# Performance work log

Measured on AMD Instinct MI355X. Metric: run time of the kernel, lower is better.

## Reference

```python
import jax, jax.numpy as jnp
import numpy as np

N, LATENT, HIDDEN, OUT, B = 65536, 128, 512, 64, 1024
W_WIDTH = 4.0  # LSH bucket width params['w']


def setup_inputs() -> dict:
    key = jax.random.key(0)
    ks = jax.random.split(key, 6)
    return {
        "z": jax.random.normal(ks[0], (N, LATENT), jnp.float32),
        "W1": jax.random.normal(ks[1], (LATENT, HIDDEN), jnp.float32) / np.float32(np.sqrt(LATENT)),
        "b1": jnp.zeros((HIDDEN,), jnp.float32),
        "W2": jax.random.normal(ks[2], (HIDDEN, OUT), jnp.float32) / np.float32(np.sqrt(HIDDEN)),
        "b2": jnp.zeros((OUT,), jnp.float32),
        "a": jax.random.normal(ks[3], (OUT,), jnp.float32),
        "lsh_b": jax.random.uniform(ks[4], (1,), jnp.float32) * W_WIDTH,
    }


def reference(z, W1, b1, W2, b2, a, lsh_b):
    # decoder MLP: latent -> hidden (relu) -> output_dim
    h = jax.nn.relu(z @ W1 + b1)
    x = h @ W2 + b2                                     # [N, OUT]
    # LSH random-projection hash: floor((x.a + b)/w), bucketed mod B
    code = jnp.floor((x @ a + lsh_b[0]) / W_WIDTH)
    bucket = jnp.mod(code.astype(jnp.int32), B)         # [N] segment ids
    # dict-based cluster grouping -> segmented mean per hash bucket
    sums = jax.ops.segment_sum(x, bucket, num_segments=B)                # [B, OUT]
    counts = jax.ops.segment_sum(jnp.ones((x.shape[0],), x.dtype), bucket, num_segments=B)
    means = sums / jnp.maximum(counts, 1.0)[:, None]    # [B, OUT]
    # squared distances point -> every cluster mean (gram trick, no [N,B,OUT] tensor)
    d2 = jnp.maximum(
        jnp.sum(x * x, -1)[:, None] + jnp.sum(means * means, -1)[None, :]
        - 2.0 * (x @ means.T),
        0.0)                                            # [N, B]
    # DEC-style Student-t soft cluster assignment
    q = 1.0 / (1.0 + d2)
    q_s = q / jnp.sum(q, -1, keepdims=True)
    return (q_s, means)
```

## Files before the change

### kernel.cpp

```cpp
#include <hip/hip_runtime.h>
#include <hip/hip_bf16.h>

#define N_PTS   65536
#define LATENT  128
#define HIDDEN  512
#define OUT_D   64
#define NBUCKET 1024
#define ROWS_A  32

typedef __attribute__((ext_vector_type(8))) short frag_ab;
typedef __attribute__((ext_vector_type(4))) float f32x4;

__device__ __forceinline__ short bf16h(float f) {
    union { float f; unsigned u; } c; c.f = f;
    const unsigned r = (c.u + 0x7FFFu + ((c.u >> 16) & 1u)) >> 16;
    return (short)r;
}
__device__ __forceinline__ float bf16tof(short s) {
    union { unsigned u; float f; } c; c.u = ((unsigned)(unsigned short)s) << 16;
    return c.f;
}

__global__ __launch_bounds__(256) void prep_weights(
    const float* __restrict__ W1, const float* __restrict__ W2,
    short* __restrict__ wfrag)
{
    const int tid = blockIdx.x * 256 + threadIdx.x;
    const int c = tid / 1536;
    const int u = tid % 1536;
    frag_ab hi, lo;
    if (u < 1024) {
        const int l = u >> 4, slot = u & 15;
        const int j = slot ^ (l & 7);
        const int ct = j >> 3, ks = (j >> 1) & 3, hl = j & 1;
        const int n = (c * 2 + ct) * 16 + (l & 15);
        const int k0 = ks * 32 + ((l >> 4) << 3);
#pragma unroll
        for (int e = 0; e < 8; ++e) {
            const float wv = W1[(size_t)(k0 + e) * HIDDEN + n];
            const short h = bf16h(wv);
            hi[e] = h;
            lo[e] = bf16h(wv - bf16tof(h));
        }
        ((frag_ab*)wfrag)[(size_t)c * 1536 + u] = hl ? lo : hi;
    } else {
        const int u2 = u - 1024;
        const int l = u2 >> 3, slot = u2 & 7;
        const int j = slot ^ (l & 7);
        const int ot = j >> 1, hl = j & 1;
        const int n = ot * 16 + (l & 15);
#pragma unroll
        for (int e = 0; e < 8; ++e) {
            const int k = c * 32 + ((e >> 2) << 4) + ((l >> 4) << 2) + (e & 3);
            const float wv = W2[(size_t)k * OUT_D + n];
            const short h = bf16h(wv);
            hi[e] = h;
            lo[e] = bf16h(wv - bf16tof(h));
        }
        ((frag_ab*)wfrag)[(size_t)c * 1536 + u] = hl ? lo : hi;
    }
}

#define BAND_U   5e-4f

__global__ __launch_bounds__(256, 2) void mlp_mfma_kernel(
    const float* __restrict__ z, const short* __restrict__ wfrag,
    const float* __restrict__ b1, const float* __restrict__ b2,
    const float* __restrict__ a, const float* __restrict__ lsh_b,
    float* __restrict__ x_out, float* __restrict__ xnorm_out,
    int* __restrict__ bucket_out, int* __restrict__ wsflag)
{
    __shared__ frag_ab LD[3072];
    float* LDf = (float*)LD;
    float4* LDf4 = (float4*)LD;
    const int t = threadIdx.x;
    const int l = t & 63, w = t >> 6;
    const int sw = l & 7;
    const int row0 = blockIdx.x * 128 + w * 32;
    const frag_ab* wg = (const frag_ab*)wfrag;

    frag_ab zh[2][4], zl[2][4];
#pragma unroll
    for (int rg = 0; rg < 2; ++rg)
#pragma unroll
        for (int ks = 0; ks < 4; ++ks) {
            const float* src = z + (size_t)(row0 + rg * 16 + (l & 15)) * LATENT
                             + ks * 32 + ((l >> 4) << 3);
            const float4 p0 = *(const float4*)src;
            const float4 p1 = *(const float4*)(src + 4);
            const float v[8] = {p0.x, p0.y, p0.z, p0.w, p1.x, p1.y, p1.z, p1.w};
#pragma unroll
            for (int e = 0; e < 8; ++e) {
                const short h = bf16h(v[e]);
                zh[rg][ks][e] = h;
                zl[rg][ks][e] = bf16h(v[e] - bf16tof(h));
            }
        }

    f32x4 acc2[2][4];
#pragma unroll
    for (int rg = 0; rg < 2; ++rg)
#pragma unroll
        for (int ot = 0; ot < 4; ++ot) acc2[rg][ot] = (f32x4){0.f, 0.f, 0.f, 0.f};

#pragma unroll
    for (int i = 0; i < 6; ++i)
        __builtin_amdgcn_global_load_lds(
            (const __attribute__((address_space(1))) void*)(wg + (w * 6 + i) * 64 + l),
            (__attribute__((address_space(3))) void*)(&LD[(w * 6 + i) * 64]),
            16, 0, 0);
    __syncthreads();

#pragma unroll 1
    for (int c = 0; c < 16; ++c) {
        const int pb = (c & 1) * 1536;
        const int sb = 1536 - pb;
        if (c < 15) {
#pragma unroll
            for (int i = 0; i < 6; ++i)
                __builtin_amdgcn_global_load_lds(
                    (const __attribute__((address_space(1))) void*)(wg + (size_t)(c + 1) * 1536 + (w * 6 + i) * 64 + l),
                    (__attribute__((address_space(3))) void*)(&LD[sb + (w * 6 + i) * 64]),
                    16, 0, 0);
        }

        f32x4 acc1[2][2];
#pragma unroll
        for (int ct_l = 0; ct_l < 2; ++ct_l) {
            frag_ab bh[4], bl[4];
#pragma unroll
            for (int ks = 0; ks < 4; ++ks) {
                bh[ks] = LD[pb + l * 16 + ct_l * 8 + ((ks * 2) ^ sw)];
                bl[ks] = LD[pb + l * 16 + ct_l * 8 + ((ks * 2 + 1) ^ sw)];
            }
#pragma unroll
            for (int rg = 0; rg < 2; ++rg) {
                f32x4 acc = (f32x4){0.f, 0.f, 0.f, 0.f};
#pragma unroll
                for (int ks = 0; ks < 4; ++ks) {
                    acc = __builtin_amdgcn_mfma_f32_16x16x32_bf16(bh[ks], zh[rg][ks], acc, 0, 0, 0);
                    acc = __builtin_amdgcn_mfma_f32_16x16x32_bf16(bl[ks], zh[rg][ks], acc, 0, 0, 0);
                    acc = __builtin_amdgcn_mfma_f32_16x16x32_bf16(bh[ks], zl[rg][ks], acc, 0, 0, 0);
                }
                acc1[ct_l][rg] = acc;
            }
        }

        float4 b1v[2];
#pragma unroll
        for (int ct_l = 0; ct_l < 2; ++ct_l)
            b1v[ct_l] = *(const float4*)&b1[(c * 2 + ct_l) * 16 + ((l >> 4) << 2)];
        frag_ab ah2[2], al2[2];
#pragma unroll
        for (int rg = 0; rg < 2; ++rg)
#pragma unroll
            for (int e = 0; e < 8; ++e) {
                const int tile = e >> 2, r = e & 3;
                const float bb = (r == 0) ? b1v[tile].x : (r == 1) ? b1v[tile].y
                               : (r == 2) ? b1v[tile].z : b1v[tile].w;
                const float hv = fmaxf(acc1[tile][rg][r] + bb, 0.f);
                const short hh = bf16h(hv);
                ah2[rg][e] = hh;
                al2[rg][e] = bf16h(hv - bf16tof(hh));
            }

#pragma unroll
        for (int ot = 0; ot < 4; ++ot) {
            const frag_ab b2h = LD[pb + 1024 + l * 8 + ((ot * 2) ^ sw)];
            const frag_ab b2l = LD[pb + 1024 + l * 8 + ((ot * 2 + 1) ^ sw)];
#pragma unroll
            for (int rg = 0; rg < 2; ++rg) {
                acc2[rg][ot] = __builtin_amdgcn_mfma_f32_16x16x32_bf16(ah2[rg], b2h, acc2[rg][ot], 0, 0, 0);
                acc2[rg][ot] = __builtin_amdgcn_mfma_f32_16x16x32_bf16(al2[rg], b2h, acc2[rg][ot], 0, 0, 0);
                acc2[rg][ot] = __builtin_amdgcn_mfma_f32_16x16x32_bf16(ah2[rg], b2l, acc2[rg][ot], 0, 0, 0);
            }
        }
        __syncthreads();
    }

    float b2v[4], av[4];
#pragma unroll
    for (int ot = 0; ot < 4; ++ot) {
        b2v[ot] = b2[ot * 16 + (l & 15)];
        av[ot]  = a[ot * 16 + (l & 15)];
    }
    const int pbase = w * 512;
    int flagged = 0;
    const float lb = lsh_b[0];
#pragma unroll
    for (int rg = 0; rg < 2; ++rg)
#pragma unroll
        for (int r = 0; r < 4; ++r) {
            float sp = 0.f, np = 0.f;
            const int row_l = rg * 16 + (l >> 4) * 4 + r;
#pragma unroll
            for (int ot = 0; ot < 4; ++ot) {
                const float xv = acc2[rg][ot][r] + b2v[ot];
                sp = fmaf(xv, av[ot], sp);
                np = fmaf(xv, xv, np);
                const int col = ot * 16 + (l & 15);
                LDf[pbase * 4 + row_l * 64 + col] = xv;
            }
#pragma unroll
            for (int off = 8; off >= 1; off >>= 1) {
                sp += __shfl_xor(sp, off, 16);
                np += __shfl_xor(np, off, 16);
            }
            if ((l & 15) == 0) {
                const int row = row0 + row_l;
                const float v = sp + lb;
                const float u = v * 0.25f;
                const float fl = floorf(u);
                bucket_out[row] = ((int)fl) & (NBUCKET - 1);
                xnorm_out[row] = np;
                const float fr = u - fl;
                if (fr < BAND_U || fr > 1.f - BAND_U) flagged = 1;
            }
        }
    const unsigned long long fb = __ballot(flagged != 0);
    if (l == 0) wsflag[blockIdx.x * 4 + w] = (fb != 0ull) ? 1 : 0;

    float4* xo4 = (float4*)x_out;
#pragma unroll
    for (int j = 0; j < 8; ++j) {
        const int u = l + 64 * j;
        const int row = u >> 4, c4 = u & 15;
        xo4[(size_t)(row0 + row) * 16 + c4] = LDf4[pbase + row * 16 + c4];
    }
}

__global__ __launch_bounds__(256, 3) void mlp_fixup_kernel(
    const float* __restrict__ z, const float* __restrict__ W1,
    const float* __restrict__ b1, const float* __restrict__ W2,
    const float* __restrict__ b2, const float* __restrict__ a,
    const float* __restrict__ lsh_b, const int* __restrict__ wsflag,
    float* __restrict__ x_out, float* __restrict__ xnorm_out,
    int* __restrict__ bucket_out)
{
    if (wsflag[blockIdx.x] == 0) return;
    __shared__ float zt[ROWS_A][LATENT];
    __shared__ float ht[ROWS_A][256];
    const int t = threadIdx.x;
    const int row0 = blockIdx.x * ROWS_A;

    {
        const float4* z4 = reinterpret_cast<const float4*>(z + (size_t)row0 * LATENT);
        float4* zt4 = reinterpret_cast<float4*>(&zt[0][0]);
#pragma unroll
        for (int i = 0; i < 4; ++i) zt4[t + 256 * i] = z4[t + 256 * i];
    }
    __syncthreads();

    const int tx = t & 63, ty = t >> 6;
    const int txq = t & 31, tyq = t >> 5;

    float acc2[4][2];
#pragma unroll
    for (int i = 0; i < 4; ++i) { acc2[i][0] = 0.f; acc2[i][1] = 0.f; }

    for (int h = 0; h < 2; ++h) {
        float acc1[8][4];
#pragma unroll
        for (int i = 0; i < 8; ++i)
#pragma unroll
            for (int cc = 0; cc < 4; ++cc) acc1[i][cc] = 0.f;

        const int jbase = h * 256 + tx;
#pragma unroll 2
        for (int k = 0; k < LATENT; k += 4) {
            float wv[4][4];
#pragma unroll
            for (int kk = 0; kk < 4; ++kk)
#pragma unroll
                for (int cc = 0; cc < 4; ++cc)
                    wv[kk][cc] = W1[(size_t)(k + kk) * HIDDEN + jbase + 64 * cc];
            float4 zv[8];
#pragma unroll
            for (int i = 0; i < 8; ++i)
                zv[i] = *reinterpret_cast<const float4*>(&zt[ty * 8 + i][k]);
#pragma unroll
            for (int i = 0; i < 8; ++i)
#pragma unroll
                for (int cc = 0; cc < 4; ++cc) {
                    acc1[i][cc] = fmaf(zv[i].x, wv[0][cc], acc1[i][cc]);
                    acc1[i][cc] = fmaf(zv[i].y, wv[1][cc], acc1[i][cc]);
                    acc1[i][cc] = fmaf(zv[i].z, wv[2][cc], acc1[i][cc]);
                    acc1[i][cc] = fmaf(zv[i].w, wv[3][cc], acc1[i][cc]);
                }
        }
        float bb[4];
#pragma unroll
        for (int cc = 0; cc < 4; ++cc) bb[cc] = b1[jbase + 64 * cc];
#pragma unroll
        for (int i = 0; i < 8; ++i)
#pragma unroll
            for (int cc = 0; cc < 4; ++cc)
                ht[ty * 8 + i][tx + 64 * cc] = fmaxf(acc1[i][cc] + bb[cc], 0.f);
        __syncthreads();

#pragma unroll 2
        for (int k = 0; k < 256; k += 4) {
            float w2v[4][2];
#pragma unroll
            for (int kk = 0; kk < 4; ++kk) {
                w2v[kk][0] = W2[(size_t)(h * 256 + k + kk) * OUT_D + txq];
                w2v[kk][1] = W2[(size_t)(h * 256 + k + kk) * OUT_D + txq + 32];
            }
            float4 hv[4];
#pragma unroll
            for (int i = 0; i < 4; ++i)
                hv[i] = *reinterpret_cast<const float4*>(&ht[tyq * 4 + i][k]);
#pragma unroll
            for (int i = 0; i < 4; ++i)
#pragma unroll
                for (int cc = 0; cc < 2; ++cc) {
                    acc2[i][cc] = fmaf(hv[i].x, w2v[0][cc], acc2[i][cc]);
                    acc2[i][cc] = fmaf(hv[i].y, w2v[1][cc], acc2[i][cc]);
                    acc2[i][cc] = fmaf(hv[i].z, w2v[2][cc], acc2[i][cc]);
                    acc2[i][cc] = fmaf(hv[i].w, w2v[3][cc], acc2[i][cc]);
                }
        }
        __syncthreads();
    }

    const float bb0 = b2[txq], bb1 = b2[txq + 32];
    const float a0 = a[txq], a1 = a[txq + 32];
    const float lb = lsh_b[0];
#pragma unroll
    for (int i = 0; i < 4; ++i) {
        const int row = row0 + tyq * 4 + i;
        const float x0 = acc2[i][0] + bb0;
        const float x1 = acc2[i][1] + bb1;
        x_out[(size_t)row * OUT_D + txq]      = x0;
        x_out[(size_t)row * OUT_D + txq + 32] = x1;

        float sa = fmaf(x0, a0, x1 * a1);
        float sn = fmaf(x0, x0, x1 * x1);
#pragma unroll
        for (int off = 16; off >= 1; off >>= 1) {
            sa += __shfl_xor(sa, off, 32);
            sn += __shfl_xor(sn, off, 32);
        }
        if (txq == 0) {
            const float code = floorf((sa + lb) * 0.25f);
            bucket_out[row] = ((int)code) & (NBUCKET - 1);
            xnorm_out[row] = sn;
        }
    }
}

__global__ __launch_bounds__(256) void hist_kernel(
    const int* __restrict__ bucket, int* __restrict__ blockhist,
    float* __restrict__ sums)
{
    __shared__ int h[NBUCKET];
    const int t = threadIdx.x, blk = blockIdx.x;
    for (int i = t; i < NBUCKET; i += 256) h[i] = 0;
    for (int i = t; i < NBUCKET; i += 256) sums[blk * NBUCKET + i] = 0.f;
    __syncthreads();
    const int rbase = blk * 1024;
#pragma unroll
    for (int i = 0; i < 4; ++i)
        atomicAdd(&h[bucket[rbase + i * 256 + t]], 1);
    __syncthreads();
    for (int i = t; i < NBUCKET; i += 256)
        blockhist[blk * NBUCKET + i] = h[i];
}

__global__ __launch_bounds__(1024) void scan_kernel(
    const int* __restrict__ blockhist, int* __restrict__ base,
    int* __restrict__ blockbase, int* __restrict__ nzbucket,
    int* __restrict__ nzcount)
{
    __shared__ int sc[NBUCKET];
    const int b = threadIdx.x;
    int vals[64];
#pragma unroll
    for (int blk = 0; blk < 64; ++blk) vals[blk] = blockhist[blk * NBUCKET + b];
    int c = 0;
#pragma unroll
    for (int blk = 0; blk < 64; ++blk) c += vals[blk];
    sc[b] = c;
    __syncthreads();
    for (int off = 1; off < NBUCKET; off <<= 1) {
        const int add = (b >= off) ? sc[b - off] : 0;
        __syncthreads();
        sc[b] += add;
        __syncthreads();
    }
    const int offset = sc[b] - c;
    base[b] = offset;
    if (b == NBUCKET - 1) base[NBUCKET] = offset + c;
    int run = offset;
#pragma unroll
    for (int blk = 0; blk < 64; ++blk) {
        blockbase[blk * NBUCKET + b] = run;
        run += vals[blk];
    }
    __syncthreads();
    const int flag = (c > 0) ? 1 : 0;
    sc[b] = flag;
    __syncthreads();
    for (int off = 1; off < NBUCKET; off <<= 1) {
        const int add = (b >= off) ? sc[b - off] : 0;
        __syncthreads();
        sc[b] += add;
        __syncthreads();
    }
    if (flag) nzbucket[sc[b] - 1] = b;
    if (b == NBUCKET - 1) nzcount[0] = sc[NBUCKET - 1];
}

__global__ __launch_bounds__(256) void scatter_kernel(
    const int* __restrict__ bucket, const int* __restrict__ blockbase,
    int* __restrict__ order)
{
    __shared__ int lcur[NBUCKET];
    const int t = threadIdx.x, blk = blockIdx.x;
    for (int i = t; i < NBUCKET; i += 256) lcur[i] = 0;
    __syncthreads();
    const int rbase = blk * 1024;
#pragma unroll
    for (int i = 0; i < 4; ++i) {
        const int row = rbase + i * 256 + t;
        const int bk = bucket[row];
        const int r = atomicAdd(&lcur[bk], 1);
        order[blockbase[blk * NBUCKET + bk] + r] = row;
    }
}

__global__ __launch_bounds__(256) void chunksum_kernel(
    const float* __restrict__ x, const int* __restrict__ order,
    const int* __restrict__ bucket, float* __restrict__ sums)
{
    const int t = threadIdx.x, lane = t & 63, w = t >> 6;
    const int c = blockIdx.x * 4 + w;
    const int i0 = c * 64;
    const int ordv = order[i0 + lane];
    const int bktv = bucket[ordv];
    float acc = 0.f;
    int cur = __shfl(bktv, 0, 64);
#pragma unroll 8
    for (int j = 0; j < 64; ++j) {
        const int rb = __shfl(ordv, j, 64);
        const int bb = __shfl(bktv, j, 64);
        if (bb != cur) {
            atomicAdd(&sums[(size_t)cur * OUT_D + lane], acc);
            acc = 0.f; cur = bb;
        }
        acc += x[(size_t)rb * OUT_D + lane];
    }
    atomicAdd(&sums[(size_t)cur * OUT_D + lane], acc);
}

__global__ __launch_bounds__(64) void means_kernel(
    const float* __restrict__ sums, const int* __restrict__ base,
    float* __restrict__ means_out, float* __restrict__ mnorm)
{
    const int b = blockIdx.x;
    const int k = threadIdx.x;
    const int cnt = base[b + 1] - base[b];
    const float m = sums[b * OUT_D + k] / fmaxf((float)cnt, 1.0f);
    means_out[b * OUT_D + k] = m;
    float s = m * m;
#pragma unroll
    for (int off = 32; off >= 1; off >>= 1) s += __shfl_xor(s, off, 64);
    if (k == 0) mnorm[b] = s;
}

__global__ __launch_bounds__(256, 3) void q_kernel(
    const float* __restrict__ x, const float* __restrict__ xnorm,
    const float* __restrict__ means, const float* __restrict__ mnorm,
    const int* __restrict__ nzbucket, const int* __restrict__ nzcount,
    float* __restrict__ q_out)
{
    __shared__ float xr[32 * 64];
    __shared__ float qrow[4 * 1024];
    __shared__ float invv[32], flinv[32];
    const int t = threadIdx.x;
    const int row0 = blockIdx.x * 32;
    const int K = nzcount[0];

    {
        const float4* x4 = (const float4*)(x + (size_t)row0 * OUT_D);
        float4* xr4 = (float4*)xr;
        xr4[t] = x4[t];
        xr4[t + 256] = x4[t + 256];
    }
    __syncthreads();

    const int r = t >> 3;
    const int sl = t & 7;
    const float xn = xnorm[row0 + r];
    float rsum = 0.f;
    {
        const float4 xa = *(const float4*)&xr[r * 64 + sl * 8];
        const float4 xb = *(const float4*)&xr[r * 64 + sl * 8 + 4];
        for (int k = 0; k < K; ++k) {
            const int bid = nzbucket[k];
            const float4 ma = *(const float4*)&means[(size_t)bid * OUT_D + sl * 8];
            const float4 mb = *(const float4*)&means[(size_t)bid * OUT_D + sl * 8 + 4];
            float d = xa.x * ma.x + xa.y * ma.y + xa.z * ma.z + xa.w * ma.w
                    + xb.x * mb.x + xb.y * mb.y + xb.z * mb.z + xb.w * mb.w;
            d += __shfl_xor(d, 1, 8);
            d += __shfl_xor(d, 2, 8);
            d += __shfl_xor(d, 4, 8);
            const float d2 = fmaxf(xn + mnorm[bid] - 2.f * d, 0.f);
            rsum += __builtin_amdgcn_rcpf(1.f + d2);
        }
    }
    const float filler = __builtin_amdgcn_rcpf(1.f + xn);
    const float tot = fmaf((float)(NBUCKET - K), filler, rsum);
    if (sl == 0) {
        const float iv = __builtin_amdgcn_rcpf(tot);
        invv[r] = iv;
        flinv[r] = filler * iv;
    }
    __syncthreads();

#pragma unroll 1
    for (int g = 0; g < 8; ++g) {
        const int rr0 = g * 4;
#pragma unroll
        for (int i = 0; i < 4; ++i) {
            const int idx = i * 256 + t;
            const float fv = flinv[rr0 + (idx >> 8)];
            ((float4*)qrow)[idx] = (float4){fv, fv, fv, fv};
        }
        __syncthreads();
        for (int p = t; p < K * 4; p += 256) {
            const int k = p >> 2, rr = p & 3;
            const int bid = nzbucket[k];
            const float* xp = &xr[(rr0 + rr) * 64];
            const float* mp = &means[(size_t)bid * OUT_D];
            float d = 0.f;
#pragma unroll 16
            for (int e = 0; e < 64; ++e) d = fmaf(xp[e], mp[e], d);
            const float d2 = fmaxf(xnorm[row0 + rr0 + rr] + mnorm[bid] - 2.f * d, 0.f);
            qrow[rr * 1024 + bid] = __builtin_amdgcn_rcpf(1.f + d2) * invv[rr0 + rr];
        }
        __syncthreads();
#pragma unroll
        for (int i = 0; i < 4; ++i) {
            const int idx = i * 256 + t;
            const int rr = idx >> 8, c4 = idx & 255;
            ((float4*)(q_out + (size_t)(row0 + rr0 + rr) * NBUCKET))[c4] =
                ((const float4*)(qrow + rr * 1024))[c4];
        }
        __syncthreads();
    }
}

extern "C" void kernel_launch(void* const* d_in, const int* in_sizes, int n_in,
                              void* d_out, int out_size, void* d_ws, size_t ws_size,
                              hipStream_t stream) {
    const float* z    = (const float*)d_in[0];
    const float* W1   = (const float*)d_in[1];
    const float* b1   = (const float*)d_in[2];
    const float* W2   = (const float*)d_in[3];
    const float* b2   = (const float*)d_in[4];
    const float* a    = (const float*)d_in[5];
    const float* lshb = (const float*)d_in[6];

    float* q_out     = (float*)d_out;
    float* means_out = q_out + (size_t)N_PTS * NBUCKET;

    char* ws = (char*)d_ws;
    float* x      = (float*)ws;
    short* wfrag  = (short*)(x + (size_t)N_PTS * OUT_D);
    float* xnorm  = (float*)(wfrag + (size_t)16 * 1536 * 8);
    float* mnorm  = xnorm + N_PTS;
    float* sums   = mnorm + NBUCKET;
    int*   bucket = (int*)(sums + (size_t)NBUCKET * OUT_D);
    int*   order  = bucket + N_PTS;
    int*   blockhist = order + N_PTS;
    int*   blockbase = blockhist + 64 * NBUCKET;
    int*   base      = blockbase + 64 * NBUCKET;
    int*   wsflag    = base + NBUCKET + 1;
    int*   nzbucket  = wsflag + 2048;
    int*   nzcount   = nzbucket + NBUCKET;

    prep_weights<<<96, 256, 0, stream>>>(W1, W2, wfrag);
    mlp_mfma_kernel<<<N_PTS / 128, 256, 0, stream>>>(z, wfrag, b1, b2, a, lshb,
                                                     x, xnorm, bucket, wsflag);
    mlp_fixup_kernel<<<N_PTS / ROWS_A, 256, 0, stream>>>(z, W1, b1, W2, b2, a, lshb, wsflag,
                                                         x, xnorm, bucket);
    hist_kernel<<<64, 256, 0, stream>>>(bucket, blockhist, sums);
    scan_kernel<<<1, 1024, 0, stream>>>(blockhist, base, blockbase, nzbucket, nzcount);
    scatter_kernel<<<64, 256, 0, stream>>>(bucket, blockbase, order);
    chunksum_kernel<<<256, 256, 0, stream>>>(x, order, bucket, sums);
    means_kernel<<<NBUCKET, 64, 0, stream>>>(sums, base, means_out, mnorm);
    q_kernel<<<N_PTS / 32, 256, 0, stream>>>(x, xnorm, means_out, mnorm,
                                             nzbucket, nzcount, q_out);
}
```

Baseline: 207.8 us.

## Replace sort-based segment sum with LDS atomics and cache Student-t values in q_kernel

Drops the scan/scatter/chunksum pipeline that ordered rows by bucket. A simplified single-block kernel now computes per-bucket counts and a compact index for the non-empty buckets, and a new accum_kernel adds each row into a shared-memory accumulator before flushing to global sums with atomics. When the number of non-empty buckets is at most 192, q_kernel stores the Student-t values from its first pass in shared memory so the second pass can skip recomputing the 64-wide dot products. This removes a launch and the gather traffic, but adds shared memory (about 24 KB more in q_kernel, which may cut occupancy) and makes the float sums depend on atomic ordering.

```diff
diff --git a/kernel.cpp b/kernel.cpp
--- a/kernel.cpp
+++ b/kernel.cpp
@@ -7,6 +7,7 @@
 #define OUT_D   64
 #define NBUCKET 1024
 #define ROWS_A  32
+#define KACC    192
 
 typedef __attribute__((ext_vector_type(8))) short frag_ab;
 typedef __attribute__((ext_vector_type(4))) float f32x4;
@@ -367,20 +368,18 @@
         blockhist[blk * NBUCKET + i] = h[i];
 }
 
-__global__ __launch_bounds__(1024) void scan_kernel(
-    const int* __restrict__ blockhist, int* __restrict__ base,
-    int* __restrict__ blockbase, int* __restrict__ nzbucket,
-    int* __restrict__ nzcount)
+__global__ __launch_bounds__(1024) void nz_kernel(
+    const int* __restrict__ blockhist, int* __restrict__ counts,
+    int* __restrict__ kid, int* __restrict__ nzbucket, int* __restrict__ nzcount)
 {
     __shared__ int sc[NBUCKET];
     const int b = threadIdx.x;
-    int vals[64];
-#pragma unroll
-    for (int blk = 0; blk < 64; ++blk) vals[blk] = blockhist[blk * NBUCKET + b];
     int c = 0;
 #pragma unroll
-    for (int blk = 0; blk < 64; ++blk) c += vals[blk];
-    sc[b] = c;
+    for (int blk = 0; blk < 64; ++blk) c += blockhist[blk * NBUCKET + b];
+    counts[b] = c;
+    const int flag = (c > 0) ? 1 : 0;
+    sc[b] = flag;
     __syncthreads();
     for (int off = 1; off < NBUCKET; off <<= 1) {
         const int add = (b >= off) ? sc[b - off] : 0;
@@ -388,79 +387,47 @@
         sc[b] += add;
         __syncthreads();
     }
-    const int offset = sc[b] - c;
-    base[b] = offset;
-    if (b == NBUCKET - 1) base[NBUCKET] = offset + c;
-    int run = offset;
-#pragma unroll
-    for (int blk = 0; blk < 64; ++blk) {
-        blockbase[blk * NBUCKET + b] = run;
-        run += vals[blk];
-    }
-    __syncthreads();
-    const int flag = (c > 0) ? 1 : 0;
-    sc[b] = flag;
-    __syncthreads();
-    for (int off = 1; off < NBUCKET; off <<= 1) {
-        const int add = (b >= off) ? sc[b - off] : 0;
-        __syncthreads();
-        sc[b] += add;
-        __syncthreads();
-    }
+    kid[b] = flag ? (sc[b] - 1) : -1;
     if (flag) nzbucket[sc[b] - 1] = b;
     if (b == NBUCKET - 1) nzcount[0] = sc[NBUCKET - 1];
 }
 
-__global__ __launch_bounds__(256) void scatter_kernel(
-    const int* __restrict__ bucket, const int* __restrict__ blockbase,
-    int* __restrict__ order)
-{
-    __shared__ int lcur[NBUCKET];
-    const int t = threadIdx.x, blk = blockIdx.x;
-    for (int i = t; i < NBUCKET; i += 256) lcur[i] = 0;
-    __syncthreads();
-    const int rbase = blk * 1024;
-#pragma unroll
-    for (int i = 0; i < 4; ++i) {
-        const int row = rbase + i * 256 + t;
-        const int bk = bucket[row];
-        const int r = atomicAdd(&lcur[bk], 1);
-        order[blockbase[blk * NBUCKET + bk] + r] = row;
-    }
-}
-
-__global__ __launch_bounds__(256) void chunksum_kernel(
-    const float* __restrict__ x, const int* __restrict__ order,
-    const int* __restrict__ bucket, float* __restrict__ sums)
-{
+__global__ __launch_bounds__(256) void accum_kernel(
+    const float* __restrict__ x, const int* __restrict__ bucket,
+    const int* __restrict__ kid, const int* __restrict__ nzbucket,
+    const int* __restrict__ nzcount, float* __restrict__ sums)
+{
+    __shared__ float acc[KACC * 64];
     const int t = threadIdx.x, lane = t & 63, w = t >> 6;
-    const int c = blockIdx.x * 4 + w;
-    const int i0 = c * 64;
-    const int ordv = order[i0 + lane];
-    const int bktv = bucket[ordv];
-    float acc = 0.f;
-    int cur = __shfl(bktv, 0, 64);
-#pragma unroll 8
-    for (int j = 0; j < 64; ++j) {
-        const int rb = __shfl(ordv, j, 64);
-        const int bb = __shfl(bktv, j, 64);
-        if (bb != cur) {
-            atomicAdd(&sums[(size_t)cur * OUT_D + lane], acc);
-            acc = 0.f; cur = bb;
-        }
-        acc += x[(size_t)rb * OUT_D + lane];
-    }
-    atomicAdd(&sums[(size_t)cur * OUT_D + lane], acc);
+    const int K = nzcount[0];
+    const int row0 = blockIdx.x * 512;
+
+    if (K <= KACC) {
+        for (int i = t; i < K * 64; i += 256) acc[i] = 0.f;
+        __syncthreads();
+        for (int rr = w; rr < 512; rr += 4) {
+            const int row = row0 + rr;
+            const int kk = kid[bucket[row]];
+            atomicAdd(&acc[kk * 64 + lane], x[(size_t)row * OUT_D + lane]);
+        }
+        __syncthreads();
+        for (int i = t; i < K * 64; i += 256)
+            atomicAdd(&sums[(size_t)nzbucket[i >> 6] * OUT_D + (i & 63)], acc[i]);
+    } else {
+        for (int rr = w; rr < 512; rr += 4) {
+            const int row = row0 + rr;
+            atomicAdd(&sums[(size_t)bucket[row] * OUT_D + lane], x[(size_t)row * OUT_D + lane]);
+        }
+    }
 }
 
 __global__ __launch_bounds__(64) void means_kernel(
-    const float* __restrict__ sums, const int* __restrict__ base,
+    const float* __restrict__ sums, const int* __restrict__ counts,
     float* __restrict__ means_out, float* __restrict__ mnorm)
 {
     const int b = blockIdx.x;
     const int k = threadIdx.x;
-    const int cnt = base[b + 1] - base[b];
-    const float m = sums[b * OUT_D + k] / fmaxf((float)cnt, 1.0f);
+    const float m = sums[b * OUT_D + k] / fmaxf((float)counts[b], 1.0f);
     means_out[b * OUT_D + k] = m;
     float s = m * m;
 #pragma unroll
@@ -476,10 +443,12 @@
 {
     __shared__ float xr[32 * 64];
     __shared__ float qrow[4 * 1024];
+    __shared__ float qreal[32 * 193];
     __shared__ float invv[32], flinv[32];
     const int t = threadIdx.x;
     const int row0 = blockIdx.x * 32;
     const int K = nzcount[0];
+    const bool small = (K <= KACC);
 
     {
         const float4* x4 = (const float4*)(x + (size_t)row0 * OUT_D);
@@ -506,7 +475,9 @@
             d += __shfl_xor(d, 2, 8);
             d += __shfl_xor(d, 4, 8);
             const float d2 = fmaxf(xn + mnorm[bid] - 2.f * d, 0.f);
-            rsum += __builtin_amdgcn_rcpf(1.f + d2);
+            const float qv = __builtin_amdgcn_rcpf(1.f + d2);
+            rsum += qv;
+            if (small && sl == 0) qreal[r * 193 + k] = qv;
         }
     }
     const float filler = __builtin_amdgcn_rcpf(1.f + xn);
@@ -531,13 +502,19 @@
         for (int p = t; p < K * 4; p += 256) {
             const int k = p >> 2, rr = p & 3;
             const int bid = nzbucket[k];
-            const float* xp = &xr[(rr0 + rr) * 64];
-            const float* mp = &means[(size_t)bid * OUT_D];
-            float d = 0.f;
+            float qv;
+            if (small) {
+                qv = qreal[(rr0 + rr) * 193 + k];
+            } else {
+                const float* xp = &xr[(rr0 + rr) * 64];
+                const float* mp = &means[(size_t)bid * OUT_D];
+                float d = 0.f;
 #pragma unroll 16
-            for (int e = 0; e < 64; ++e) d = fmaf(xp[e], mp[e], d);
-            const float d2 = fmaxf(xnorm[row0 + rr0 + rr] + mnorm[bid] - 2.f * d, 0.f);
-            qrow[rr * 1024 + bid] = __builtin_amdgcn_rcpf(1.f + d2) * invv[rr0 + rr];
+                for (int e = 0; e < 64; ++e) d = fmaf(xp[e], mp[e], d);
+                const float d2 = fmaxf(xnorm[row0 + rr0 + rr] + mnorm[bid] - 2.f * d, 0.f);
+                qv = __builtin_amdgcn_rcpf(1.f + d2);
+            }
+            qrow[rr * 1024 + bid] = qv * invv[rr0 + rr];
         }
         __syncthreads();
 #pragma unroll
@@ -572,13 +549,12 @@
     float* mnorm  = xnorm + N_PTS;
     float* sums   = mnorm + NBUCKET;
     int*   bucket = (int*)(sums + (size_t)NBUCKET * OUT_D);
-    int*   order  = bucket + N_PTS;
-    int*   blockhist = order + N_PTS;
-    int*   blockbase = blockhist + 64 * NBUCKET;
-    int*   base      = blockbase + 64 * NBUCKET;
-    int*   wsflag    = base + NBUCKET + 1;
+    int*   blockhist = bucket + N_PTS;
+    int*   counts    = blockhist + 64 * NBUCKET;
+    int*   wsflag    = counts + NBUCKET;
     int*   nzbucket  = wsflag + 2048;
     int*   nzcount   = nzbucket + NBUCKET;
+    int*   kid       = nzcount + 16;
 
     prep_weights<<<96, 256, 0, stream>>>(W1, W2, wfrag);
     mlp_mfma_kernel<<<N_PTS / 128, 256, 0, stream>>>(z, wfrag, b1, b2, a, lshb,
@@ -586,10 +562,9 @@
     mlp_fixup_kernel<<<N_PTS / ROWS_A, 256, 0, stream>>>(z, W1, b1, W2, b2, a, lshb, wsflag,
                                                          x, xnorm, bucket);
     hist_kernel<<<64, 256, 0, stream>>>(bucket, blockhist, sums);
-    scan_kernel<<<1, 1024, 0, stream>>>(blockhist, base, blockbase, nzbucket, nzcount);
-    scatter_kernel<<<64, 256, 0, stream>>>(bucket, blockbase, order);
-    chunksum_kernel<<<256, 256, 0, stream>>>(x, order, bucket, sums);
-    means_kernel<<<NBUCKET, 64, 0, stream>>>(sums, base, means_out, mnorm);
+    nz_kernel<<<1, 1024, 0, stream>>>(blockhist, counts, kid, nzbucket, nzcount);
+    accum_kernel<<<N_PTS / 512, 256, 0, stream>>>(x, bucket, kid, nzbucket, nzcount, sums);
+    means_kernel<<<NBUCKET, 64, 0, stream>>>(sums, counts, means_out, mnorm);
     q_kernel<<<N_PTS / 32, 256, 0, stream>>>(x, xnorm, means_out, mnorm,
                                              nzbucket, nzcount, q_out);
 }
```

Result: slower. 240.9 us (+15.9%).
